# Kernel tuning notes

Hardware: AMD Instinct MI355X
Metric: run time of the kernel (lower is better)

## Reference

```python
import jax, jax.numpy as jnp
import numpy as np

DIM, NH, T_MAX = 1024, 16, 2048
HD = DIM // NH
EPS = 1e-6


def _rope_tables(T, hd, dtype=jnp.float32):
    inv_freq = 1.0 / (10000.0 ** (jnp.arange(0, hd, 2, dtype=jnp.float32) / hd))
    t = jnp.arange(T, dtype=jnp.float32)
    freqs = jnp.outer(t, inv_freq)                 # [T, hd/2]
    emb = jnp.concatenate([freqs, freqs], axis=-1)  # [T, hd]
    return jnp.cos(emb).astype(dtype), jnp.sin(emb).astype(dtype)


def _rotate_half(x):
    x1, x2 = jnp.split(x, 2, axis=-1)
    return jnp.concatenate([-x2, x1], axis=-1)


def _rmsnorm(x, g):
    rms = jnp.sqrt(jnp.mean(x * x, axis=-1, keepdims=True) + EPS)
    return x / rms * g


def setup_inputs() -> dict:
    key = jax.random.key(0)
    ks = jax.random.split(key, 10)
    B, T, C = 4, 2048, DIM
    s = 1.0 / np.sqrt(C)
    x = jax.random.normal(ks[0], (B, T, C), dtype=jnp.float32)
    mask = jnp.tril(jnp.ones((T, T), dtype=jnp.int32))[None, None, :, :]
    wq = jax.random.normal(ks[1], (C, C), jnp.float32) * s
    wk = jax.random.normal(ks[2], (C, C), jnp.float32) * s
    wv = jax.random.normal(ks[3], (C, C), jnp.float32) * s
    wo = jax.random.normal(ks[4], (C, C), jnp.float32) * s
    w1 = jax.random.normal(ks[5], (C, 4 * C), jnp.float32) * s
    w2 = jax.random.normal(ks[6], (4 * C, C), jnp.float32) * (1.0 / np.sqrt(4 * C))
    w3 = jax.random.normal(ks[7], (C, 4 * C), jnp.float32) * s
    g1 = jnp.ones((C,), jnp.float32)
    g2 = jnp.ones((C,), jnp.float32)
    return {"x": x, "mask": mask, "g1": g1, "wq": wq, "wk": wk, "wv": wv,
            "wo": wo, "g2": g2, "w1": w1, "w2": w2, "w3": w3}


def reference(x, mask, g1, wq, wk, wv, wo, g2, w1, w2, w3):
    B, T, C = x.shape
    scale = HD ** -0.5
    # --- attention sublayer ---
    h = _rmsnorm(x, g1)
    q = (h @ wq).reshape(B, T, NH, HD)
    k = (h @ wk).reshape(B, T, NH, HD)
    v = (h @ wv).reshape(B, T, NH, HD)
    cos, sin = _rope_tables(T, HD, x.dtype)
    cos = cos[None, :, None, :]
    sin = sin[None, :, None, :]
    q = q * cos + _rotate_half(q) * sin
    k = k * cos + _rotate_half(k) * sin
    attn = jnp.einsum("bthd,bshd->bhts", q, k) * scale  # [B,H,T,T]
    attn = jnp.where(mask == 0, -jnp.inf, attn)
    attn = jax.nn.softmax(attn, axis=-1)
    o = jnp.einsum("bhts,bshd->bthd", attn, v).reshape(B, T, C)
    x = x + o @ wo
    # --- SwiGLU FFN sublayer ---
    h = _rmsnorm(x, g2)
    x = x + (jax.nn.silu(h @ w1) * (h @ w3)) @ w2
    return x
```

## Files before the change

kernel.cpp:

```cpp
#include <hip/hip_runtime.h>
#include <cstdint>

typedef unsigned short u16;
typedef __attribute__((ext_vector_type(8))) short bf16x8;
typedef __attribute__((ext_vector_type(4))) float f32x4;

__device__ __forceinline__ u16 f2b(float f) {
  union { float f; unsigned u; } c; c.f = f;
  unsigned u = c.u;
  return (u16)((u + 0x7FFFu + ((u >> 16) & 1u)) >> 16);
}
__device__ __forceinline__ float b2f(u16 b) {
  union { unsigned u; float f; } c; c.u = ((unsigned)b) << 16;
  return c.f;
}

typedef __attribute__((address_space(1))) void gv_t;
typedef __attribute__((address_space(3))) void lv_t;
__device__ __forceinline__ void gload_lds16(const void* g, void* l) {
  __builtin_amdgcn_global_load_lds((gv_t*)g, (lv_t*)l, 16, 0, 0);
}

__global__ void transpose_f2b(const float* __restrict__ in, u16* __restrict__ out,
                              int R, int C) {
  __shared__ float t[32][33];
  const int c0 = blockIdx.x * 32, r0 = blockIdx.y * 32;
  const int tx = threadIdx.x, ty = threadIdx.y;
#pragma unroll
  for (int i = 0; i < 4; ++i)
    t[ty + 8 * i][tx] = in[(size_t)(r0 + ty + 8 * i) * C + c0 + tx];
  __syncthreads();
#pragma unroll
  for (int i = 0; i < 4; ++i)
    out[(size_t)(c0 + ty + 8 * i) * R + r0 + tx] = f2b(t[tx][ty + 8 * i]);
}

__global__ __launch_bounds__(256) void rmsnorm_k(const float* __restrict__ x,
                                                 const float* __restrict__ g,
                                                 u16* __restrict__ out) {
  const int row = blockIdx.x, tid = threadIdx.x;
  const float4 v = ((const float4*)x)[(size_t)row * 256 + tid];
  float ss = v.x * v.x + v.y * v.y + v.z * v.z + v.w * v.w;
#pragma unroll
  for (int off = 1; off < 64; off <<= 1) ss += __shfl_xor(ss, off, 64);
  __shared__ float red[4];
  if ((tid & 63) == 0) red[tid >> 6] = ss;
  __syncthreads();
  const float mean = (red[0] + red[1] + red[2] + red[3]) * (1.0f / 1024.0f);
  const float rinv = 1.0f / sqrtf(mean + 1e-6f);
  const float4 gv = ((const float4*)g)[tid];
  u16* o = out + (size_t)row * 1024 + tid * 4;
  o[0] = f2b(v.x * rinv * gv.x);
  o[1] = f2b(v.y * rinv * gv.y);
  o[2] = f2b(v.z * rinv * gv.z);
  o[3] = f2b(v.w * rinv * gv.w);
}

__global__ __launch_bounds__(256) void rope_k(u16* __restrict__ qkv) {
  const int i = blockIdx.x * 256 + threadIdx.x;
  const int d = i & 31;
  const int h = (i >> 5) & 15;
  const int bt = i >> 9;
  const int t = bt & 2047;
  const float inv = exp2f((float)d * -0.4152410118609203f);
  const float th = (float)t * inv;
  float s, c;
  sincosf(th, &s, &c);
  size_t base = (size_t)bt * 3072 + h * 64 + d;
#pragma unroll
  for (int half = 0; half < 2; ++half) {
    const float x1 = b2f(qkv[base]);
    const float x2 = b2f(qkv[base + 32]);
    qkv[base]      = f2b(x1 * c - x2 * s);
    qkv[base + 32] = f2b(x2 * c + x1 * s);
    base += 1024;
  }
}

__global__ void vtrans_k(const u16* __restrict__ qkv, u16* __restrict__ VT) {
  __shared__ u16 tl[32][34];
  const int t0 = blockIdx.x * 32;
  const int bh = blockIdx.y >> 1;
  const int d0 = (blockIdx.y & 1) * 32;
  const int b = bh >> 4, h = bh & 15;
  const int tx = threadIdx.x, ty = threadIdx.y;
  const u16* src = qkv + (size_t)(b * 2048 + t0) * 3072 + 2048 + h * 64 + d0;
#pragma unroll
  for (int i = 0; i < 4; ++i)
    tl[ty + 8 * i][tx] = src[(size_t)(ty + 8 * i) * 3072 + tx];
  __syncthreads();
  u16* dst = VT + ((size_t)bh * 64 + d0) * 2048 + t0;
#pragma unroll
  for (int i = 0; i < 4; ++i)
    dst[(size_t)(ty + 8 * i) * 2048 + tx] = tl[tx][ty + 8 * i];
}

template <int EPI>
__global__ __launch_bounds__(256)
void gemm_bt(const u16* __restrict__ A, const u16* __restrict__ BT,
             void* __restrict__ Cout, const float* __restrict__ resid,
             int M, int N, int K, int lda) {
  __shared__ alignas(16) u16 As[128 * 32];
  __shared__ alignas(16) u16 Bs[128 * 32];
  const int tid = threadIdx.x;
  const int wave = tid >> 6, lane = tid & 63;
  const int wr = wave >> 1, wc = wave & 1;
  const int l15 = lane & 15, quad = lane >> 4;
  const int bm = blockIdx.x * 128, bn = blockIdx.y * 128;

  f32x4 acc[4][4];
#pragma unroll
  for (int i = 0; i < 4; ++i)
#pragma unroll
    for (int j = 0; j < 4; ++j) acc[i][j] = (f32x4){0.f, 0.f, 0.f, 0.f};

  const int srow = wave * 32 + (lane >> 2);
  const int scol = (lane & 3) * 8;
  const u16* gA0 = A + (size_t)(bm + srow) * lda + scol;
  const u16* gA1 = gA0 + (size_t)16 * lda;
  const u16* gB0 = BT + (size_t)(bn + srow) * K + scol;
  const u16* gB1 = gB0 + (size_t)16 * K;
  u16* lA0 = As + wave * 1024; u16* lA1 = lA0 + 512;
  u16* lB0 = Bs + wave * 1024; u16* lB1 = lB0 + 512;

  const u16* pa = As + (wr * 64 + l15) * 32 + quad * 8;
  const u16* pb = Bs + (wc * 64 + l15) * 32 + quad * 8;

  for (int kt = 0; kt < K; kt += 32) {
    gload_lds16(gA0 + kt, lA0);
    gload_lds16(gA1 + kt, lA1);
    gload_lds16(gB0 + kt, lB0);
    gload_lds16(gB1 + kt, lB1);
    __syncthreads();
    bf16x8 af[4], bfv[4];
#pragma unroll
    for (int i = 0; i < 4; ++i) af[i] = *(const bf16x8*)(pa + i * 512);
#pragma unroll
    for (int j = 0; j < 4; ++j) bfv[j] = *(const bf16x8*)(pb + j * 512);
#pragma unroll
    for (int i = 0; i < 4; ++i)
#pragma unroll
      for (int j = 0; j < 4; ++j)
        acc[i][j] = __builtin_amdgcn_mfma_f32_16x16x32_bf16(af[i], bfv[j], acc[i][j], 0, 0, 0);
    __syncthreads();
  }

#pragma unroll
  for (int i = 0; i < 4; ++i) {
    const int gr = bm + wr * 64 + i * 16 + quad * 4;
#pragma unroll
    for (int j = 0; j < 4; ++j) {
      const int gc = bn + wc * 64 + j * 16 + l15;
#pragma unroll
      for (int r = 0; r < 4; ++r) {
        const size_t off = (size_t)(gr + r) * N + gc;
        if (EPI == 0) {
          ((u16*)Cout)[off] = f2b(acc[i][j][r]);
        } else {
          ((float*)Cout)[off] = resid[off] + acc[i][j][r];
        }
      }
    }
  }
}

template <int EPI>
__global__ __launch_bounds__(512, 2)
void gemm256(const u16* __restrict__ A, const u16* __restrict__ BT,
             void* __restrict__ Cout, const float* __restrict__ resid,
             int M, int N, int K, int lda) {
  __shared__ alignas(16) u16 LDS[65536];
  char* const ldsc = (char*)LDS;
  const int tid = threadIdx.x;
  const int wave = tid >> 6, lane = tid & 63;
  const int wr = wave >> 2, wc = wave & 3;
  const int l15 = lane & 15, quad = lane >> 4;
  const int bm = blockIdx.x * 256, bn = blockIdx.y * 256;
  const int NT = K >> 6;
  const int NIT = NT >> 1;

  const int swz = (l15 & 8) << 2;
  const int aoff = (((wr * 64 + l15) * 64 + quad * 16) ^ swz);
  const int boff = (((wc * 32 + l15) * 64 + quad * 16) ^ swz) + 65536;

  const int kperm = ((lane & 3) ^ ((lane >> 5) << 1)) * 8;
  const u16* sA = A + (size_t)(bm + wave * 16 + (lane >> 2)) * lda + kperm;
  const u16* sB = BT + (size_t)(bn + wave * 16 + (lane >> 2)) * K + kperm;
  const size_t hA = (size_t)128 * lda;
  const size_t hB = (size_t)128 * K;
  const int dstW = wave * 1024;

  f32x4 acc[8][4];
#pragma unroll
  for (int m = 0; m < 8; ++m)
#pragma unroll
    for (int n = 0; n < 4; ++n) acc[m][n] = (f32x4){0.f, 0.f, 0.f, 0.f};
  bf16x8 a[4][2], b[2][2];

#define STAGE(kt_, slot_, buf_)                                               \
  if ((kt_) < NT) {                                                           \
    const u16* s_ = (((slot_) & 1) ? sB + ((size_t)((slot_) >> 1)) * hB       \
                                   : sA + ((size_t)((slot_) >> 1)) * hA) +    \
                    (size_t)(kt_) * 64;                                       \
    char* d_ = ldsc + (((slot_) & 1) ? 65536 : 0) + (buf_) * 32768 +          \
               ((slot_) >> 1) * 16384 + dstW;                                 \
    gload_lds16(s_, d_);                                                      \
    gload_lds16(s_ + 32, d_ + 8192);                                          \
  }

#define LOAD_A(mh_, buf_)                                                     \
  _Pragma("unroll") for (int mf = 0; mf < 4; ++mf)                            \
      _Pragma("unroll") for (int kk = 0; kk < 2; ++kk)                        \
          a[mf][kk] = *(const bf16x8*)(ldsc + aoff + (buf_) * 32768 +         \
                                       (mh_) * 16384 + kk * 8192 + mf * 1024);

#define LOAD_B(nh_, buf_)                                                     \
  _Pragma("unroll") for (int nf = 0; nf < 2; ++nf)                            \
      _Pragma("unroll") for (int kk = 0; kk < 2; ++kk)                        \
          b[nf][kk] = *(const bf16x8*)(ldsc + boff + (buf_) * 32768 +         \
                                       (nh_) * 16384 + kk * 8192 + nf * 1024);

#define MMA(mh_, nh_)                                                         \
  __builtin_amdgcn_s_setprio(1);                                              \
  _Pragma("unroll") for (int mf = 0; mf < 4; ++mf)                            \
      _Pragma("unroll") for (int nf = 0; nf < 2; ++nf)                        \
          _Pragma("unroll") for (int kk = 0; kk < 2; ++kk)                    \
              acc[(mh_) * 4 + mf][(nh_) * 2 + nf] =                           \
                  __builtin_amdgcn_mfma_f32_16x16x32_bf16(                    \
                      a[mf][kk], b[nf][kk],                                   \
                      acc[(mh_) * 4 + mf][(nh_) * 2 + nf], 0, 0, 0);          \
  __builtin_amdgcn_s_setprio(0);

#define BAR() __builtin_amdgcn_s_barrier()
#define DRAIN_LGKM()                                                          \
  {                                                                           \
    asm volatile("s_waitcnt lgkmcnt(0)" ::: "memory");                        \
    __builtin_amdgcn_sched_barrier(0);                                        \
  }

  STAGE(0, 0, 0); STAGE(0, 1, 0); STAGE(0, 2, 0); STAGE(0, 3, 0);
  STAGE(1, 0, 1); STAGE(1, 1, 1);
  asm volatile("s_waitcnt vmcnt(4)" ::: "memory");
  BAR();

  for (int i = 0; i < NIT; ++i) {
    const int t = 2 * i;
    LOAD_A(0, 0); LOAD_B(0, 0); STAGE(t + 1, 2, 1);
    BAR(); DRAIN_LGKM(); MMA(0, 0); BAR();
    LOAD_B(1, 0); STAGE(t + 1, 3, 1);
    BAR(); DRAIN_LGKM(); MMA(0, 1); BAR();
    LOAD_A(1, 0); LOAD_B(0, 0); STAGE(t + 2, 0, 0);
    BAR(); DRAIN_LGKM(); MMA(1, 0); BAR();
    LOAD_B(1, 0); STAGE(t + 2, 1, 0);
    BAR(); DRAIN_LGKM(); MMA(1, 1);
    if (i == NIT - 1) { asm volatile("s_waitcnt vmcnt(0)" ::: "memory"); }
    else              { asm volatile("s_waitcnt vmcnt(4)" ::: "memory"); }
    BAR();
    LOAD_A(0, 1); LOAD_B(0, 1); STAGE(t + 2, 2, 0);
    BAR(); DRAIN_LGKM(); MMA(0, 0); BAR();
    LOAD_B(1, 1); STAGE(t + 2, 3, 0);
    BAR(); DRAIN_LGKM(); MMA(0, 1); BAR();
    LOAD_A(1, 1); LOAD_B(0, 1); STAGE(t + 3, 0, 1);
    BAR(); DRAIN_LGKM(); MMA(1, 0); BAR();
    LOAD_B(1, 1); STAGE(t + 3, 1, 1);
    BAR(); DRAIN_LGKM(); MMA(1, 1);
    if (i < NIT - 1) { asm volatile("s_waitcnt vmcnt(4)" ::: "memory"); }
    BAR();
  }
#undef STAGE
#undef LOAD_A
#undef LOAD_B
#undef MMA
#undef BAR
#undef DRAIN_LGKM

#pragma unroll
  for (int m = 0; m < 8; ++m) {
    const int gr = bm + (m >> 2) * 128 + wr * 64 + (m & 3) * 16 + quad * 4;
#pragma unroll
    for (int n = 0; n < 4; ++n) {
      const int gc = bn + (n >> 1) * 128 + wc * 32 + (n & 1) * 16 + l15;
#pragma unroll
      for (int r = 0; r < 4; ++r) {
        const size_t off = (size_t)(gr + r) * N + gc;
        if (EPI == 0) {
          ((u16*)Cout)[off] = f2b(acc[m][n][r]);
        } else {
          ((float*)Cout)[off] = resid[off] + acc[m][n][r];
        }
      }
    }
  }
}

__global__ __launch_bounds__(256)
void attn_kernel(const u16* __restrict__ QKV, const u16* __restrict__ VT,
                 u16* __restrict__ O) {
  const int T = 2048, stQ = 3072;
  const int tid = threadIdx.x, wave = tid >> 6, lane = tid & 63;
  const int l15 = lane & 15, quad = lane >> 4;
  const int qt = (int)gridDim.x - 1 - (int)blockIdx.x;
  const int qb0 = qt * 128;
  const int bh = blockIdx.y, b = bh >> 4, h = bh & 15;
  const float sc2 = 0.125f * 1.44269504088896f;
  const float M0 = 32.0f;

  __shared__ alignas(16) u16 Kf[8 * 512];
  __shared__ alignas(16) u16 Vf[8 * 512];
  __shared__ alignas(16) u16 Pl[4][2][16 * 72];

  const u16* Qb  = QKV + (size_t)b * T * stQ + h * 64;
  const u16* Kb  = Qb + 1024;
  const u16* VTb = VT + (size_t)bh * 64 * T;

  const int r0 = qb0 + wave * 16;
  const int r1 = r0 + 64;
  const u16* qp0 = Qb + (size_t)(r0 + l15) * stQ + quad * 8;
  const u16* qp1 = Qb + (size_t)(r1 + l15) * stQ + quad * 8;
  const bf16x8 qf00 = *(const bf16x8*)qp0;
  const bf16x8 qf01 = *(const bf16x8*)(qp0 + 32);
  const bf16x8 qf10 = *(const bf16x8*)qp1;
  const bf16x8 qf11 = *(const bf16x8*)(qp1 + 32);

  bf16x8 ones;
#pragma unroll
  for (int j = 0; j < 8; ++j) ones[j] = (short)0x3F80;

  const u16* kS = Kb + (size_t)(wave * 16 + l15) * stQ + quad * 8;
  const u16* vS = VTb + (size_t)(wave * 16 + l15) * T + quad * 8;
  u16* kD0 = Kf + (wave * 2 + 0) * 512;  u16* kD1 = Kf + (wave * 2 + 1) * 512;
  u16* vD0 = Vf + (wave * 2 + 0) * 512;  u16* vD1 = Vf + (wave * 2 + 1) * 512;

  f32x4 o0[4], o1[4], sum0, sum1;
#pragma unroll
  for (int c = 0; c < 4; ++c) {
    o0[c] = (f32x4){0.f, 0.f, 0.f, 0.f};
    o1[c] = (f32x4){0.f, 0.f, 0.f, 0.f};
  }
  sum0 = (f32x4){0.f, 0.f, 0.f, 0.f};
  sum1 = (f32x4){0.f, 0.f, 0.f, 0.f};

  u16* pw0 = &Pl[wave][0][0];
  u16* pw1 = &Pl[wave][1][0];

  const int nkt = qt * 2 + 2;
  for (int kt = 0; kt < nkt; ++kt) {
    const int kb0 = kt * 64;
    gload_lds16(kS + (size_t)kb0 * stQ,      kD0);
    gload_lds16(kS + (size_t)kb0 * stQ + 32, kD1);
    gload_lds16(vS + kb0,                    vD0);
    gload_lds16(vS + kb0 + 32,               vD1);
    __syncthreads();

    bf16x8 kf[8];
#pragma unroll
    for (int g = 0; g < 8; ++g)
      kf[g] = *(const bf16x8*)(Kf + g * 512 + lane * 8);

    const bool act0 = (kb0 <= r0 + 15);

    {
      f32x4 s[4];
#pragma unroll
      for (int jj = 0; jj < 4; ++jj) {
        s[jj] = (f32x4){0.f, 0.f, 0.f, 0.f};
        s[jj] = __builtin_amdgcn_mfma_f32_16x16x32_bf16(qf10, kf[jj * 2 + 0], s[jj], 0, 0, 0);
        s[jj] = __builtin_amdgcn_mfma_f32_16x16x32_bf16(qf11, kf[jj * 2 + 1], s[jj], 0, 0, 0);
      }
      if (kb0 + 63 > r1) {
#pragma unroll
        for (int jj = 0; jj < 4; ++jj)
#pragma unroll
          for (int r = 0; r < 4; ++r) {
            const bool msk = (kb0 + jj * 16 + l15) > (r1 + quad * 4 + r);
            const float a = msk ? -1e30f : (s[jj][r] * sc2 - M0);
            pw1[(quad * 4 + r) * 72 + jj * 16 + l15] = f2b(exp2f(a));
          }
      } else {
#pragma unroll
        for (int jj = 0; jj < 4; ++jj)
#pragma unroll
          for (int r = 0; r < 4; ++r)
            pw1[(quad * 4 + r) * 72 + jj * 16 + l15] =
                f2b(exp2f(s[jj][r] * sc2 - M0));
      }
    }
    if (act0) {
      f32x4 s[4];
#pragma unroll
      for (int jj = 0; jj < 4; ++jj) {
        s[jj] = (f32x4){0.f, 0.f, 0.f, 0.f};
        s[jj] = __builtin_amdgcn_mfma_f32_16x16x32_bf16(qf00, kf[jj * 2 + 0], s[jj], 0, 0, 0);
        s[jj] = __builtin_amdgcn_mfma_f32_16x16x32_bf16(qf01, kf[jj * 2 + 1], s[jj], 0, 0, 0);
      }
      if (kb0 + 63 > r0) {
#pragma unroll
        for (int jj = 0; jj < 4; ++jj)
#pragma unroll
          for (int r = 0; r < 4; ++r) {
            const bool msk = (kb0 + jj * 16 + l15) > (r0 + quad * 4 + r);
            const float a = msk ? -1e30f : (s[jj][r] * sc2 - M0);
            pw0[(quad * 4 + r) * 72 + jj * 16 + l15] = f2b(exp2f(a));
          }
      } else {
#pragma unroll
        for (int jj = 0; jj < 4; ++jj)
#pragma unroll
          for (int r = 0; r < 4; ++r)
            pw0[(quad * 4 + r) * 72 + jj * 16 + l15] =
                f2b(exp2f(s[jj][r] * sc2 - M0));
      }
    }

    const bf16x8 pf10 = *(const bf16x8*)(pw1 + l15 * 72 + quad * 8);
    const bf16x8 pf11 = *(const bf16x8*)(pw1 + l15 * 72 + 32 + quad * 8);
#pragma unroll
    for (int c = 0; c < 4; ++c) {
      const bf16x8 v0 = *(const bf16x8*)(Vf + (c * 2 + 0) * 512 + lane * 8);
      const bf16x8 v1 = *(const bf16x8*)(Vf + (c * 2 + 1) * 512 + lane * 8);
      o1[c] = __builtin_amdgcn_mfma_f32_16x16x32_bf16(pf10, v0, o1[c], 0, 0, 0);
      o1[c] = __builtin_amdgcn_mfma_f32_16x16x32_bf16(pf11, v1, o1[c], 0, 0, 0);
    }
    sum1 = __builtin_amdgcn_mfma_f32_16x16x32_bf16(pf10, ones, sum1, 0, 0, 0);
    sum1 = __builtin_amdgcn_mfma_f32_16x16x32_bf16(pf11, ones, sum1, 0, 0, 0);
    if (act0) {
      const bf16x8 pf00 = *(const bf16x8*)(pw0 + l15 * 72 + quad * 8);
      const bf16x8 pf01 = *(const bf16x8*)(pw0 + l15 * 72 + 32 + quad * 8);
#pragma unroll
      for (int c = 0; c < 4; ++c) {
        const bf16x8 v0 = *(const bf16x8*)(Vf + (c * 2 + 0) * 512 + lane * 8);
        const bf16x8 v1 = *(const bf16x8*)(Vf + (c * 2 + 1) * 512 + lane * 8);
        o0[c] = __builtin_amdgcn_mfma_f32_16x16x32_bf16(pf00, v0, o0[c], 0, 0, 0);
        o0[c] = __builtin_amdgcn_mfma_f32_16x16x32_bf16(pf01, v1, o0[c], 0, 0, 0);
      }
      sum0 = __builtin_amdgcn_mfma_f32_16x16x32_bf16(pf00, ones, sum0, 0, 0, 0);
      sum0 = __builtin_amdgcn_mfma_f32_16x16x32_bf16(pf01, ones, sum0, 0, 0, 0);
    }
    __syncthreads();
  }

  float i0[4], i1[4];
#pragma unroll
  for (int r = 0; r < 4; ++r) { i0[r] = 1.f / sum0[r]; i1[r] = 1.f / sum1[r]; }
  u16* op0 = O + ((size_t)(b * T) + r0 + quad * 4) * 1024 + h * 64 + l15;
  u16* op1 = O + ((size_t)(b * T) + r1 + quad * 4) * 1024 + h * 64 + l15;
#pragma unroll
  for (int c = 0; c < 4; ++c)
#pragma unroll
    for (int r = 0; r < 4; ++r) {
      op0[(size_t)r * 1024 + c * 16] = f2b(o0[c][r] * i0[r]);
      op1[(size_t)r * 1024 + c * 16] = f2b(o1[c][r] * i1[r]);
    }
}

__global__ __launch_bounds__(256) void gate_k(u16* __restrict__ a13) {
  const size_t i = (size_t)blockIdx.x * 256 + threadIdx.x;
  const size_t row = i >> 9, c8 = (i & 511) * 8;
  u16* p1v = a13 + row * 8192 + c8;
  const u16* p3v = p1v + 4096;
  uint4 u1 = *(uint4*)p1v;
  const uint4 u3 = *(const uint4*)p3v;
  u16* p1 = (u16*)&u1;
  const u16* p3 = (const u16*)&u3;
#pragma unroll
  for (int j = 0; j < 8; ++j) {
    const float a = b2f(p1[j]);
    const float g = b2f(p3[j]);
    const float s = a / (1.f + __expf(-a));
    p1[j] = f2b(s * g);
  }
  *(uint4*)p1v = u1;
}

extern "C" void kernel_launch(void* const* d_in, const int* in_sizes, int n_in,
                              void* d_out, int out_size, void* d_ws, size_t ws_size,
                              hipStream_t stream) {
  const float* x  = (const float*)d_in[0];
  const float* g1 = (const float*)d_in[2];
  const float* wq = (const float*)d_in[3];
  const float* wk = (const float*)d_in[4];
  const float* wv = (const float*)d_in[5];
  const float* wo = (const float*)d_in[6];
  const float* g2 = (const float*)d_in[7];
  const float* w1 = (const float*)d_in[8];
  const float* w2 = (const float*)d_in[9];
  const float* w3 = (const float*)d_in[10];
  float* out = (float*)d_out;

  const int T = 2048, NH = 16, B = 4;
  const int M = B * T;
  const size_t MB = 1ull << 20;

  char* ws = (char*)d_ws;
  u16* hb    = (u16*)(ws);
  u16* wqkvT = (u16*)(ws + 16 * MB);
  u16* woT   = (u16*)(ws + 22 * MB);
  u16* w13T  = (u16*)(ws + 24 * MB);
  u16* w2T   = (u16*)(ws + 40 * MB);
  u16* qkv   = (u16*)(ws + 48 * MB);
  u16* VT    = (u16*)(ws + 96 * MB);
  u16* Ob    = (u16*)(ws + 112 * MB);
  u16* a13   = (u16*)(ws + 48 * MB);

  const dim3 tb(32, 8);
  transpose_f2b<<<dim3(32, 32),  tb, 0, stream>>>(wq, wqkvT,              1024, 1024);
  transpose_f2b<<<dim3(32, 32),  tb, 0, stream>>>(wk, wqkvT + 1024*1024,  1024, 1024);
  transpose_f2b<<<dim3(32, 32),  tb, 0, stream>>>(wv, wqkvT + 2048*1024,  1024, 1024);
  transpose_f2b<<<dim3(32, 32),  tb, 0, stream>>>(wo, woT, 1024, 1024);
  transpose_f2b<<<dim3(128, 32), tb, 0, stream>>>(w1, w13T,               1024, 4096);
  transpose_f2b<<<dim3(128, 32), tb, 0, stream>>>(w3, w13T + 4096*1024,   1024, 4096);
  transpose_f2b<<<dim3(32, 128), tb, 0, stream>>>(w2, w2T, 4096, 1024);

  rmsnorm_k<<<M, 256, 0, stream>>>(x, g1, hb);

  gemm256<0><<<dim3(32, 12), 512, 0, stream>>>(hb, wqkvT, qkv, nullptr, M, 3072, 1024, 1024);

  rope_k<<<16384, 256, 0, stream>>>(qkv);
  vtrans_k<<<dim3(64, 128), tb, 0, stream>>>(qkv, VT);

  attn_kernel<<<dim3(T / 128, B * NH), 256, 0, stream>>>(qkv, VT, Ob);

  gemm_bt<1><<<dim3(64, 8), 256, 0, stream>>>(Ob, woT, out, x, M, 1024, 1024, 1024);

  rmsnorm_k<<<M, 256, 0, stream>>>(out, g2, hb);

  gemm256<0><<<dim3(32, 32), 512, 0, stream>>>(hb, w13T, a13, nullptr, M, 8192, 1024, 1024);

  gate_k<<<16384, 256, 0, stream>>>(a13);

  gemm_bt<1><<<dim3(64, 8), 256, 0, stream>>>(a13, w2T, out, out, M, 1024, 4096, 8192);
}
```

Measured before the change: 722.7 us.

## Double-buffer K/V tiles in attention with async prefetch and MFMA priority

The attention kernel now keeps two LDS buffers for K and V and issues the global-to-LDS loads for the next key tile before computing on the current one. It waits on vmcnt for only the current tile, so load latency overlaps with compute. V fragments are hoisted into registers once per tile, and s_setprio raises wave priority around the MFMA blocks. The cost is double the K/V LDS footprint, more registers, and reliance on hand-placed waitcnt and barrier ordering.

```diff
diff --git a/kernel.cpp b/kernel.cpp
--- a/kernel.cpp
+++ b/kernel.cpp
@@ -305,8 +305,8 @@
   const float sc2 = 0.125f * 1.44269504088896f;
   const float M0 = 32.0f;
 
-  __shared__ alignas(16) u16 Kf[8 * 512];
-  __shared__ alignas(16) u16 Vf[8 * 512];
+  __shared__ alignas(16) u16 Kf[2][8 * 512];
+  __shared__ alignas(16) u16 Vf[2][8 * 512];
   __shared__ alignas(16) u16 Pl[4][2][16 * 72];
 
   const u16* Qb  = QKV + (size_t)b * T * stQ + h * 64;
@@ -328,8 +328,6 @@
 
   const u16* kS = Kb + (size_t)(wave * 16 + l15) * stQ + quad * 8;
   const u16* vS = VTb + (size_t)(wave * 16 + l15) * T + quad * 8;
-  u16* kD0 = Kf + (wave * 2 + 0) * 512;  u16* kD1 = Kf + (wave * 2 + 1) * 512;
-  u16* vD0 = Vf + (wave * 2 + 0) * 512;  u16* vD1 = Vf + (wave * 2 + 1) * 512;
 
   f32x4 o0[4], o1[4], sum0, sum1;
 #pragma unroll
@@ -344,29 +342,48 @@
   u16* pw1 = &Pl[wave][1][0];
 
   const int nkt = qt * 2 + 2;
+
+  gload_lds16(kS,      &Kf[0][(wave * 2 + 0) * 512]);
+  gload_lds16(kS + 32, &Kf[0][(wave * 2 + 1) * 512]);
+  gload_lds16(vS,      &Vf[0][(wave * 2 + 0) * 512]);
+  gload_lds16(vS + 32, &Vf[0][(wave * 2 + 1) * 512]);
+
   for (int kt = 0; kt < nkt; ++kt) {
     const int kb0 = kt * 64;
-    gload_lds16(kS + (size_t)kb0 * stQ,      kD0);
-    gload_lds16(kS + (size_t)kb0 * stQ + 32, kD1);
-    gload_lds16(vS + kb0,                    vD0);
-    gload_lds16(vS + kb0 + 32,               vD1);
-    __syncthreads();
-
-    bf16x8 kf[8];
-#pragma unroll
-    for (int g = 0; g < 8; ++g)
-      kf[g] = *(const bf16x8*)(Kf + g * 512 + lane * 8);
+    const int buf = kt & 1;
+    __builtin_amdgcn_sched_barrier(0);
+    if (kt + 1 < nkt) {
+      const size_t kb1 = (size_t)(kb0 + 64);
+      gload_lds16(kS + kb1 * stQ,      &Kf[buf ^ 1][(wave * 2 + 0) * 512]);
+      gload_lds16(kS + kb1 * stQ + 32, &Kf[buf ^ 1][(wave * 2 + 1) * 512]);
+      gload_lds16(vS + kb1,            &Vf[buf ^ 1][(wave * 2 + 0) * 512]);
+      gload_lds16(vS + kb1 + 32,       &Vf[buf ^ 1][(wave * 2 + 1) * 512]);
+      asm volatile("s_waitcnt vmcnt(4)" ::: "memory");
+    } else {
+      asm volatile("s_waitcnt vmcnt(0)" ::: "memory");
+    }
+    __builtin_amdgcn_s_barrier();
+    __builtin_amdgcn_sched_barrier(0);
+
+    bf16x8 kf[8], vf[8];
+#pragma unroll
+    for (int g = 0; g < 8; ++g) {
+      kf[g] = *(const bf16x8*)(&Kf[buf][g * 512 + lane * 8]);
+      vf[g] = *(const bf16x8*)(&Vf[buf][g * 512 + lane * 8]);
+    }
 
     const bool act0 = (kb0 <= r0 + 15);
 
     {
       f32x4 s[4];
+      __builtin_amdgcn_s_setprio(1);
 #pragma unroll
       for (int jj = 0; jj < 4; ++jj) {
         s[jj] = (f32x4){0.f, 0.f, 0.f, 0.f};
         s[jj] = __builtin_amdgcn_mfma_f32_16x16x32_bf16(qf10, kf[jj * 2 + 0], s[jj], 0, 0, 0);
         s[jj] = __builtin_amdgcn_mfma_f32_16x16x32_bf16(qf11, kf[jj * 2 + 1], s[jj], 0, 0, 0);
       }
+      __builtin_amdgcn_s_setprio(0);
       if (kb0 + 63 > r1) {
 #pragma unroll
         for (int jj = 0; jj < 4; ++jj)
@@ -387,12 +404,14 @@
     }
     if (act0) {
       f32x4 s[4];
+      __builtin_amdgcn_s_setprio(1);
 #pragma unroll
       for (int jj = 0; jj < 4; ++jj) {
         s[jj] = (f32x4){0.f, 0.f, 0.f, 0.f};
         s[jj] = __builtin_amdgcn_mfma_f32_16x16x32_bf16(qf00, kf[jj * 2 + 0], s[jj], 0, 0, 0);
         s[jj] = __builtin_amdgcn_mfma_f32_16x16x32_bf16(qf01, kf[jj * 2 + 1], s[jj], 0, 0, 0);
       }
+      __builtin_amdgcn_s_setprio(0);
       if (kb0 + 63 > r0) {
 #pragma unroll
         for (int jj = 0; jj < 4; ++jj)
@@ -414,29 +433,29 @@
 
     const bf16x8 pf10 = *(const bf16x8*)(pw1 + l15 * 72 + quad * 8);
     const bf16x8 pf11 = *(const bf16x8*)(pw1 + l15 * 72 + 32 + quad * 8);
+    __builtin_amdgcn_s_setprio(1);
 #pragma unroll
     for (int c = 0; c < 4; ++c) {
-      const bf16x8 v0 = *(const bf16x8*)(Vf + (c * 2 + 0) * 512 + lane * 8);
-      const bf16x8 v1 = *(const bf16x8*)(Vf + (c * 2 + 1) * 512 + lane * 8);
-      o1[c] = __builtin_amdgcn_mfma_f32_16x16x32_bf16(pf10, v0, o1[c], 0, 0, 0);
-      o1[c] = __builtin_amdgcn_mfma_f32_16x16x32_bf16(pf11, v1, o1[c], 0, 0, 0);
+      o1[c] = __builtin_amdgcn_mfma_f32_16x16x32_bf16(pf10, vf[c * 2 + 0], o1[c], 0, 0, 0);
+      o1[c] = __builtin_amdgcn_mfma_f32_16x16x32_bf16(pf11, vf[c * 2 + 1], o1[c], 0, 0, 0);
     }
     sum1 = __builtin_amdgcn_mfma_f32_16x16x32_bf16(pf10, ones, sum1, 0, 0, 0);
     sum1 = __builtin_amdgcn_mfma_f32_16x16x32_bf16(pf11, ones, sum1, 0, 0, 0);
+    __builtin_amdgcn_s_setprio(0);
     if (act0) {
       const bf16x8 pf00 = *(const bf16x8*)(pw0 + l15 * 72 + quad * 8);
       const bf16x8 pf01 = *(const bf16x8*)(pw0 + l15 * 72 + 32 + quad * 8);
+      __builtin_amdgcn_s_setprio(1);
 #pragma unroll
       for (int c = 0; c < 4; ++c) {
-        const bf16x8 v0 = *(const bf16x8*)(Vf + (c * 2 + 0) * 512 + lane * 8);
-        const bf16x8 v1 = *(const bf16x8*)(Vf + (c * 2 + 1) * 512 + lane * 8);
-        o0[c] = __builtin_amdgcn_mfma_f32_16x16x32_bf16(pf00, v0, o0[c], 0, 0, 0);
-        o0[c] = __builtin_amdgcn_mfma_f32_16x16x32_bf16(pf01, v1, o0[c], 0, 0, 0);
+        o0[c] = __builtin_amdgcn_mfma_f32_16x16x32_bf16(pf00, vf[c * 2 + 0], o0[c], 0, 0, 0);
+        o0[c] = __builtin_amdgcn_mfma_f32_16x16x32_bf16(pf01, vf[c * 2 + 1], o0[c], 0, 0, 0);
       }
       sum0 = __builtin_amdgcn_mfma_f32_16x16x32_bf16(pf00, ones, sum0, 0, 0, 0);
       sum0 = __builtin_amdgcn_mfma_f32_16x16x32_bf16(pf01, ones, sum0, 0, 0, 0);
-    }
-    __syncthreads();
+      __builtin_amdgcn_s_setprio(0);
+    }
+    __builtin_amdgcn_s_barrier();
   }
 
   float i0[4], i1[4];
```

After: 723.1 us. About the same (+0.1%).
